# Kernel optimization log

Hardware: AMD Instinct MI355X
Metric: run time of the kernel (lower is better)

The kernel has to match this reference:

```python
import jax, jax.numpy as jnp
import numpy as np

B, T, V, E, H, L = 32, 128, 32000, 1024, 1024, 3


def lstm_layer(x, Wx, Wh, b, h0, c0):
    """Standard LSTM (i,f,g,o gate order). x: [B,T,D]. Returns ([B,T,H], (h,c))."""
    def step(carry, xt):
        h, c = carry
        z = xt @ Wx + h @ Wh + b          # [B, 4H]
        i, f, g, o = jnp.split(z, 4, axis=-1)
        c = jax.nn.sigmoid(f) * c + jax.nn.sigmoid(i) * jnp.tanh(g)
        h = jax.nn.sigmoid(o) * jnp.tanh(c)
        return (h, c), h
    (h, c), ys = jax.lax.scan(step, (h0, c0), jnp.swapaxes(x, 0, 1))
    return jnp.swapaxes(ys, 0, 1), (h, c)


def setup_inputs() -> dict:
    key = jax.random.key(0)
    ks = jax.random.split(key, 12)
    s = 0.05  # small init to avoid gate saturation
    inp = {
        "enc_ids": jax.random.randint(ks[0], (B, T), 0, V, dtype=jnp.int32),
        "dec_ids": jax.random.randint(ks[1], (B, T), 0, V, dtype=jnp.int32),
        "emb": jax.random.normal(ks[2], (V, E), jnp.float32) * s,
        "Wx_enc": jax.random.normal(ks[3], (L, E, 4 * H), jnp.float32) * s,
        "Wh_enc": jax.random.normal(ks[4], (L, H, 4 * H), jnp.float32) * s,
        "b_enc": jnp.zeros((L, 4 * H), jnp.float32),
        "Wx_dec": jax.random.normal(ks[5], (L, E, 4 * H), jnp.float32) * s,
        "Wh_dec": jax.random.normal(ks[6], (L, H, 4 * H), jnp.float32) * s,
        "b_dec": jnp.zeros((L, 4 * H), jnp.float32),
        "dense_W": jax.random.normal(ks[7], (H, V), jnp.float32) * s,
        "dense_b": jnp.zeros((V,), jnp.float32),
    }
    return inp


def reference(enc_ids, dec_ids, emb, Wx_enc, Wh_enc, b_enc, Wx_dec, Wh_dec, b_dec, dense_W, dense_b):
    zeros = jnp.zeros((B, H), jnp.float32)
    # encoder: 3 stacked LSTMs, zero initial state each
    x = emb[enc_ids]                                      # [B,T,E]
    state = (zeros, zeros)
    for l in range(L):
        x, state = lstm_layer(x, Wx_enc[l], Wh_enc[l], b_enc[l], zeros, zeros)
    # decoder: faithful to source state chaining:
    # dec layer0 init = enc layer2 final; dec layer_{i+1} init = dec layer_i final
    y = emb[dec_ids]                                      # [B,T,E]
    for l in range(L):
        y, state = lstm_layer(y, Wx_dec[l], Wh_dec[l], b_dec[l], state[0], state[1])
    logits = y.reshape(-1, H) @ dense_W + dense_b          # [B*T, V]
    return logits.reshape(B, T, V)
```

## Files before the change

kernel.cpp:

```cpp
#include <hip/hip_runtime.h>


typedef __bf16 bf8 __attribute__((ext_vector_type(8)));
typedef float  f4  __attribute__((ext_vector_type(4)));

#define TLEN  128
#define HID   1024
#define G4    4096
#define VOC   32000
#define NBLK_SEQ 64

__device__ __forceinline__ ushort f2bf(float f) {
  unsigned u = __builtin_bit_cast(unsigned, f);
  u += 0x7fffu + ((u >> 16) & 1u);
  return (ushort)(u >> 16);
}
__device__ __forceinline__ float sigmoidf_(float x) { return 1.f / (1.f + expf(-x)); }

__device__ __forceinline__ void ld16_sys(uint4& v, const void* p) {
  asm volatile("global_load_dwordx4 %0, %1, off sc0 sc1" : "=v"(v) : "v"(p));
}
__device__ __forceinline__ unsigned ld4_sys(const void* p) {
  unsigned v;
  asm volatile("global_load_dword %0, %1, off sc0 sc1\n\ts_waitcnt vmcnt(0)"
               : "=v"(v) : "v"(p) : "memory");
  return v;
}
__device__ __forceinline__ void ld4_sys3(unsigned& a, unsigned& b, unsigned& c,
                                         const void* pa, const void* pb, const void* pc) {
  asm volatile("global_load_dword %0, %3, off sc0 sc1\n\t"
               "global_load_dword %1, %4, off sc0 sc1\n\t"
               "global_load_dword %2, %5, off sc0 sc1\n\t"
               "s_waitcnt vmcnt(0)"
               : "=&v"(a), "=&v"(b), "=&v"(c)
               : "v"(pa), "v"(pb), "v"(pc) : "memory");
}
__device__ __forceinline__ void st4_sys(void* p, unsigned v) {
  asm volatile("global_store_dword %0, %1, off sc0 sc1" :: "v"(p), "v"(v) : "memory");
}
__device__ __forceinline__ void wait_vm0() {
  asm volatile("s_waitcnt vmcnt(0)" ::: "memory");
  __builtin_amdgcn_sched_barrier(0);
}

typedef const __attribute__((address_space(1))) void GvoidC;
typedef __attribute__((address_space(3))) void Lvoid;
__device__ __forceinline__ void g2l16(const void* g, void* l) {
  __builtin_amdgcn_global_load_lds((GvoidC*)g, (Lvoid*)l, 16, 0, 0);
}

__global__ __launch_bounds__(256) void embed_kernel(const int* __restrict__ ids,
    const float* __restrict__ emb, ushort* __restrict__ out) {
  int r = blockIdx.x;
  int b = r & 31, t = r >> 5;
  int id = ids[b * TLEN + t];
  const float4* src = (const float4*)(emb + (size_t)id * HID);
  float4 v = src[threadIdx.x];
  ushort4 o;
  o.x = f2bf(v.x); o.y = f2bf(v.y); o.z = f2bf(v.z); o.w = f2bf(v.w);
  *(ushort4*)(out + (size_t)r * HID + threadIdx.x * 4) = o;
}

__global__ __launch_bounds__(256) void transpose_cvt(const float* __restrict__ W,
    ushort* __restrict__ Wt, int R, int C) {
  __shared__ float tile[32][33];
  int tx = threadIdx.x & 31, ty = threadIdx.x >> 5;
  int c0 = blockIdx.x * 32, r0 = blockIdx.y * 32;
  #pragma unroll
  for (int i = 0; i < 32; i += 8)
    tile[ty + i][tx] = W[(size_t)(r0 + ty + i) * C + c0 + tx];
  __syncthreads();
  #pragma unroll
  for (int i = 0; i < 32; i += 8)
    Wt[(size_t)(c0 + ty + i) * R + r0 + tx] = f2bf(tile[tx][ty + i]);
}

__global__ __launch_bounds__(256) void gemm_bt(const ushort* __restrict__ A,
    const ushort* __restrict__ Bt, const float* __restrict__ bias,
    float* __restrict__ C, int M, int N, int K, int permute) {
  __shared__ __align__(16) ushort lA[2 * 128 * 32];
  __shared__ __align__(16) ushort lB[2 * 128 * 32];
  int tid = threadIdx.x;
  int lane = tid & 63, wave = tid >> 6;
  int nwg = gridDim.x * gridDim.y;
  int wg  = blockIdx.y * gridDim.x + blockIdx.x;
  int q   = nwg >> 3;
  int swg = (wg & 7) * q + (wg >> 3);
  int m0 = (swg / gridDim.x) * 128, n0 = (swg % gridDim.x) * 128;
  int wr = wave >> 1, wc = wave & 1;
  f4 zero = {0.f, 0.f, 0.f, 0.f};
  f4 acc[4][4];
  #pragma unroll
  for (int i = 0; i < 4; i++)
    #pragma unroll
    for (int j = 0; j < 4; j++) acc[i][j] = zero;

  const ushort* Ag = A  + (size_t)(m0 + wave * 32 + (lane >> 2)) * K + (lane & 3) * 8;
  const ushort* Bg = Bt + (size_t)(n0 + wave * 32 + (lane >> 2)) * K + (lane & 3) * 8;
  ushort* lApa = lA + wave * 1024;
  ushort* lApb = lA + 4096 + wave * 1024;
  ushort* lBpa = lB + wave * 1024;
  ushort* lBpb = lB + 4096 + wave * 1024;

  for (int kt = 0; kt < K; kt += 64) {
    g2l16(Ag + kt,                    lApa);
    g2l16(Ag + (size_t)16 * K + kt,       lApa + 512);
    g2l16(Ag + kt + 32,               lApb);
    g2l16(Ag + (size_t)16 * K + kt + 32,  lApb + 512);
    g2l16(Bg + kt,                    lBpa);
    g2l16(Bg + (size_t)16 * K + kt,       lBpa + 512);
    g2l16(Bg + kt + 32,               lBpb);
    g2l16(Bg + (size_t)16 * K + kt + 32,  lBpb + 512);
    __syncthreads();
    #pragma unroll
    for (int h = 0; h < 2; h++) {
      const ushort* ab = lA + h * 4096;
      const ushort* bb = lB + h * 4096;
      bf8 aF[4], bF[4];
      #pragma unroll
      for (int i = 0; i < 4; i++)
        aF[i] = *(const bf8*)(ab + (wr * 64 + i * 16 + (lane & 15)) * 32 + (lane >> 4) * 8);
      #pragma unroll
      for (int j = 0; j < 4; j++)
        bF[j] = *(const bf8*)(bb + (wc * 64 + j * 16 + (lane & 15)) * 32 + (lane >> 4) * 8);
      #pragma unroll
      for (int i = 0; i < 4; i++)
        #pragma unroll
        for (int j = 0; j < 4; j++)
          acc[i][j] = __builtin_amdgcn_mfma_f32_16x16x32_bf16(aF[i], bF[j], acc[i][j], 0, 0, 0);
    }
    __syncthreads();
  }
  #pragma unroll
  for (int i = 0; i < 4; i++) {
    #pragma unroll
    for (int j = 0; j < 4; j++) {
      int col = n0 + wc * 64 + j * 16 + (lane & 15);
      float bv = bias ? bias[col] : 0.f;
      #pragma unroll
      for (int v = 0; v < 4; v++) {
        int row = m0 + wr * 64 + i * 16 + (lane >> 4) * 4 + v;
        int orow = permute ? ((row & 31) * TLEN + (row >> 5)) : row;
        C[(size_t)orow * N + col] = acc[i][j][v] + bv;
      }
    }
  }
}

__global__ __launch_bounds__(512, 1) void enc_wave(
    const float*  __restrict__ Zpre,
    const ushort* __restrict__ WhT,
    const ushort* __restrict__ WxT,
    const float*  __restrict__ bE,
    ushort*       __restrict__ hxC,
    float*        __restrict__ cSe,
    ushort*       __restrict__ hS,
    unsigned*     __restrict__ flags)
{
  const int bx = blockIdx.x;
  const int l = bx >> 6, jg = bx & 63;
  const int j0 = jg * 16;
  const int tid = threadIdx.x;
  const int lane = tid & 63, wave = tid >> 6;
  const int op = wave >> 2, ks = wave & 3;
  const int rr = tid >> 4, jj = tid & 15;

  __shared__ float zp[8][4][32][17];

  float cc = cSe[(size_t)l * 32768 + rr * HID + j0 + jj];
  float bias4[4];
  #pragma unroll
  for (int g = 0; g < 4; g++)
    bias4[g] = bE[l * G4 + g * HID + j0 + jj];

  const bool mfma_on = (l > 0) || (op == 0);
  bf8 bw[4][8];
  if (mfma_on) {
    const ushort* Wb = op ? (WxT + (size_t)(l - 1) * G4 * HID)
                          : (WhT + (size_t)l * G4 * HID);
    #pragma unroll
    for (int g = 0; g < 4; g++) {
      const ushort* Bp = Wb + (size_t)(g * HID + j0 + (lane & 15)) * HID
                       + ks * 256 + (lane >> 4) * 8;
      #pragma unroll
      for (int kk = 0; kk < 8; kk++)
        bw[g][kk] = *(const bf8*)(Bp + kk * 32);
    }
  }

  const int r0 = lane & 15, r1 = r0 + 16;
  const int lk = lane >> 4;
  const int aoff0 = ks * 8192 + (lk >> 1) * 512 + r0 * 16 + (lk & 1) * 8;
  const int aoff1 = ks * 8192 + (lk >> 1) * 512 + r1 * 16 + (lk & 1) * 8;

  float zv4[4], zn4[4];
  if (l == 0) {
    #pragma unroll
    for (int g = 0; g < 4; g++)
      zv4[g] = Zpre[(size_t)rr * G4 + g * HID + j0 + jj];
  }

  for (int w = 0; w < 130; ++w) {
    if (w > 0) {
      if (wave == 0) {
        for (;;) {
          unsigned a, b, c;
          ld4_sys3(a, b, c, flags + lane * 4, flags + (64 + lane) * 4,
                   flags + (128 + lane) * 4);
          if (!__ballot(a < (unsigned)w || b < (unsigned)w || c < (unsigned)w)) break;
          __builtin_amdgcn_s_sleep(1);
        }
      }
      __syncthreads();
    }
    const int t = w - l;
    if (t >= 0 && t < TLEN) {
      uint4 ha0[8], ha1[8];
      if (mfma_on) {
        const ushort* src = (op == 0)
          ? hxC + ((size_t)l * 2 + ((t - 1) & 1)) * 32768
          : hxC + ((size_t)(l - 1) * 2 + (t & 1)) * 32768;
        #pragma unroll
        for (int kk = 0; kk < 8; kk++) {
          ld16_sys(ha0[kk], src + aoff0 + kk * 1024);
          ld16_sys(ha1[kk], src + aoff1 + kk * 1024);
        }
        wait_vm0();
      }

      if (l == 0 && t + 1 < TLEN) {
        const float* Ztn = Zpre + (size_t)(t + 1) * 32 * G4;
        #pragma unroll
        for (int g = 0; g < 4; g++)
          zn4[g] = Ztn[(size_t)rr * G4 + g * HID + j0 + jj];
      }

      if (mfma_on) {
        f4 acc0[4], acc1[4];
        #pragma unroll
        for (int g = 0; g < 4; g++) { acc0[g] = (f4){0,0,0,0}; acc1[g] = (f4){0,0,0,0}; }
        #pragma unroll
        for (int kk = 0; kk < 8; kk++) {
          bf8 a0 = __builtin_bit_cast(bf8, ha0[kk]);
          bf8 a1 = __builtin_bit_cast(bf8, ha1[kk]);
          #pragma unroll
          for (int g = 0; g < 4; g++) {
            acc0[g] = __builtin_amdgcn_mfma_f32_16x16x32_bf16(a0, bw[g][kk], acc0[g], 0, 0, 0);
            acc1[g] = __builtin_amdgcn_mfma_f32_16x16x32_bf16(a1, bw[g][kk], acc1[g], 0, 0, 0);
          }
        }
        #pragma unroll
        for (int g = 0; g < 4; g++)
          #pragma unroll
          for (int v = 0; v < 4; v++) {
            zp[wave][g][(lane >> 4) * 4 + v][lane & 15]      = acc0[g][v];
            zp[wave][g][16 + (lane >> 4) * 4 + v][lane & 15] = acc1[g][v];
          }
      }
      __syncthreads();

      float z[4];
      #pragma unroll
      for (int g = 0; g < 4; g++) {
        float s = zp[0][g][rr][jj] + zp[1][g][rr][jj]
                + zp[2][g][rr][jj] + zp[3][g][rr][jj];
        if (l > 0)
          s += zp[4][g][rr][jj] + zp[5][g][rr][jj]
             + zp[6][g][rr][jj] + zp[7][g][rr][jj] + bias4[g];
        else
          s += zv4[g];
        z[g] = s;
      }
      if (l == 0) {
        #pragma unroll
        for (int g = 0; g < 4; g++) zv4[g] = zn4[g];
      }
      float ig = sigmoidf_(z[0]), fg = sigmoidf_(z[1]);
      float gv = tanhf(z[2]),     og = sigmoidf_(z[3]);
      cc = fg * cc + ig * gv;
      float hv = og * tanhf(cc);
      ushort hb = f2bf(hv);
      unsigned u = (unsigned)hb;
      unsigned nb = __shfl_xor(u, 1);
      if ((jj & 1) == 0)
        st4_sys(hxC + ((size_t)l * 2 + (t & 1)) * 32768 + jg * 512 + rr * 16 + jj,
                u | (nb << 16));
      if (t == TLEN - 1) {
        hS [(size_t)l * 32768 + rr * HID + j0 + jj] = hb;
        cSe[(size_t)l * 32768 + rr * HID + j0 + jj] = cc;
      }
      wait_vm0();
    }
    __syncthreads();
    if (tid == 0) st4_sys(flags + bx * 4, (unsigned)(w + 1));
  }
}

__global__ __launch_bounds__(256, 1) void lstm_seq(
    const float*  __restrict__ Zpre,
    const ushort* __restrict__ Wht,
    float*        __restrict__ cS,
    ushort*       __restrict__ yout,
    ushort*       __restrict__ hx,
    unsigned*     __restrict__ flags,
    unsigned fbase)
{
  const int jg = blockIdx.x;
  const int j0 = jg * 16;
  const int tid = threadIdx.x;
  const int lane = tid & 63, wave = tid >> 6;
  const int rr = tid >> 3, cp = tid & 7;

  __shared__ float zp[4][4][32][17];

  float2 cc = *(const float2*)(cS + (size_t)rr * HID + j0 + 2 * cp);

  bf8 bw[4][8];
  #pragma unroll
  for (int g = 0; g < 4; g++) {
    const ushort* Bp = Wht + (size_t)(g * HID + j0 + (lane & 15)) * HID
                     + wave * 256 + (lane >> 4) * 8;
    #pragma unroll
    for (int kk = 0; kk < 8; kk++)
      bw[g][kk] = *(const bf8*)(Bp + kk * 32);
  }

  const int r0 = lane & 15, r1 = r0 + 16;
  const int lk = lane >> 4;
  const int aoff0 = wave * 8192 + (lk >> 1) * 512 + r0 * 16 + (lk & 1) * 8;
  const int aoff1 = wave * 8192 + (lk >> 1) * 512 + r1 * 16 + (lk & 1) * 8;

  float2 zv[4], zn[4];
  #pragma unroll
  for (int g = 0; g < 4; g++)
    zv[g] = *(const float2*)(Zpre + (size_t)rr * G4 + g * HID + j0 + 2 * cp);

  for (int t = 0; t < TLEN; ++t) {
    if (t > 0) {
      const unsigned* fp = flags + lane * 4;
      const unsigned want = fbase + (unsigned)t;
      while (__ballot(ld4_sys(fp) < want)) {}
    }
    const ushort* hsrc = hx + ((t + 1) & 1) * 32768;
    uint4 ha0[8], ha1[8];
    #pragma unroll
    for (int kk = 0; kk < 8; kk++) {
      ld16_sys(ha0[kk], hsrc + aoff0 + kk * 1024);
      ld16_sys(ha1[kk], hsrc + aoff1 + kk * 1024);
    }
    wait_vm0();

    if (t + 1 < TLEN) {
      const float* Ztn = Zpre + (size_t)(t + 1) * 32 * G4;
      #pragma unroll
      for (int g = 0; g < 4; g++)
        zn[g] = *(const float2*)(Ztn + (size_t)rr * G4 + g * HID + j0 + 2 * cp);
    }

    f4 acc0[4], acc1[4];
    #pragma unroll
    for (int g = 0; g < 4; g++) { acc0[g] = (f4){0,0,0,0}; acc1[g] = (f4){0,0,0,0}; }
    #pragma unroll
    for (int kk = 0; kk < 8; kk++) {
      bf8 a0 = __builtin_bit_cast(bf8, ha0[kk]);
      bf8 a1 = __builtin_bit_cast(bf8, ha1[kk]);
      #pragma unroll
      for (int g = 0; g < 4; g++) {
        acc0[g] = __builtin_amdgcn_mfma_f32_16x16x32_bf16(a0, bw[g][kk], acc0[g], 0, 0, 0);
        acc1[g] = __builtin_amdgcn_mfma_f32_16x16x32_bf16(a1, bw[g][kk], acc1[g], 0, 0, 0);
      }
    }
    #pragma unroll
    for (int g = 0; g < 4; g++)
      #pragma unroll
      for (int v = 0; v < 4; v++) {
        zp[wave][g][(lane >> 4) * 4 + v][lane & 15]      = acc0[g][v];
        zp[wave][g][16 + (lane >> 4) * 4 + v][lane & 15] = acc1[g][v];
      }
    __syncthreads();

    float zx[4], zy[4];
    #pragma unroll
    for (int g = 0; g < 4; g++) {
      zx[g] = zv[g].x + zp[0][g][rr][2 * cp]     + zp[1][g][rr][2 * cp]
                      + zp[2][g][rr][2 * cp]     + zp[3][g][rr][2 * cp];
      zy[g] = zv[g].y + zp[0][g][rr][2 * cp + 1] + zp[1][g][rr][2 * cp + 1]
                      + zp[2][g][rr][2 * cp + 1] + zp[3][g][rr][2 * cp + 1];
    }
    cc.x = sigmoidf_(zx[1]) * cc.x + sigmoidf_(zx[0]) * tanhf(zx[2]);
    cc.y = sigmoidf_(zy[1]) * cc.y + sigmoidf_(zy[0]) * tanhf(zy[2]);
    float hv0 = sigmoidf_(zx[3]) * tanhf(cc.x);
    float hv1 = sigmoidf_(zy[3]) * tanhf(cc.y);
    unsigned packed = (unsigned)f2bf(hv0) | ((unsigned)f2bf(hv1) << 16);
    *(unsigned*)(yout + (size_t)t * 32768 + rr * HID + j0 + 2 * cp) = packed;
    st4_sys(hx + (size_t)(t & 1) * 32768 + jg * 512 + rr * 16 + 2 * cp, packed);
    #pragma unroll
    for (int g = 0; g < 4; g++) zv[g] = zn[g];

    wait_vm0();
    __syncthreads();
    if (tid == 0) st4_sys(flags + jg * 4, fbase + (unsigned)(t + 1));
  }
  *(float2*)(cS + (size_t)rr * HID + j0 + 2 * cp) = cc;
}

__global__ __launch_bounds__(256) void prep_enc(ushort* hxC, float* cSe,
                                                unsigned* flags) {
  int i = blockIdx.x * 256 + threadIdx.x;
  hxC[i] = 0;
  if (i < 98304) cSe[i] = 0.f;
  if (i < 192)   flags[i * 4] = 0;
}
__global__ __launch_bounds__(256) void prep_dec0(const ushort* __restrict__ hS2,
                                                 const float* __restrict__ cSe2,
                                                 float* cS, ushort* hx,
                                                 unsigned* flags) {
  int i = blockIdx.x * 256 + threadIdx.x;
  int row = i >> 10, col = i & 1023;
  hx[32768 + (col >> 4) * 512 + row * 16 + (col & 15)] = hS2[i];
  cS[i] = cSe2[i];
  if (i < NBLK_SEQ) flags[i * 4] = 0;
}

extern "C" void kernel_launch(void* const* d_in, const int* in_sizes, int n_in,
                              void* d_out, int out_size, void* d_ws, size_t ws_size,
                              hipStream_t stream) {
  const int*   enc_ids = (const int*)d_in[0];
  const int*   dec_ids = (const int*)d_in[1];
  const float* emb     = (const float*)d_in[2];
  const float* Wx_enc  = (const float*)d_in[3];
  const float* Wh_enc  = (const float*)d_in[4];
  const float* b_enc   = (const float*)d_in[5];
  const float* Wx_dec  = (const float*)d_in[6];
  const float* Wh_dec  = (const float*)d_in[7];
  const float* b_dec   = (const float*)d_in[8];
  const float* dense_W = (const float*)d_in[9];
  const float* dense_b = (const float*)d_in[10];
  float* out = (float*)d_out;

  char* ws = (char*)d_ws;
  const size_t SZ_BUF = (size_t)4096 * 1024 * 2;
  ushort*   bufA   = (ushort*)(ws);
  ushort*   bufB   = (ushort*)(ws + SZ_BUF);
  ushort*   Wxt    = (ushort*)(ws + 2 * SZ_BUF);
  ushort*   Wht    = (ushort*)(ws + 3 * SZ_BUF);
  ushort*   dWt    = (ushort*)(ws + 4 * SZ_BUF);
  char*     p2     = ws + 4 * SZ_BUF + (size_t)VOC * 1024 * 2;
  float*    cS     = (float*)(p2 + (size_t)32 * 1024 * 2);
  unsigned* flags  = (unsigned*)(p2 + (size_t)32 * 1024 * 2 + (size_t)32 * 1024 * 4);

  char* ob = (char*)d_out;
  float*    Zpre   = out;
  ushort*   WhTe   = (ushort*)(ob + (size_t)64  * 1024 * 1024);
  ushort*   WxTe   = (ushort*)(ob + (size_t)88  * 1024 * 1024);
  char*     st     = ob + (size_t)112 * 1024 * 1024;
  ushort*   hxC    = (ushort*)st;
  float*    cSe    = (float*)(st + 393216);
  ushort*   hS     = (ushort*)(st + 786432);
  unsigned* flags2 = (unsigned*)(st + 983040);
  ushort*   hxD    = (ushort*)(ob + (size_t)120 * 1024 * 1024);
  const size_t WSTRIDE = (size_t)G4 * HID;

  transpose_cvt<<<dim3(VOC / 32, 1024 / 32), 256, 0, stream>>>(dense_W, dWt, 1024, VOC);

  embed_kernel<<<4096, 256, 0, stream>>>(enc_ids, emb, bufA);
  transpose_cvt<<<dim3(G4 / 32, 32), 256, 0, stream>>>(Wx_enc, Wxt, 1024, G4);
  gemm_bt<<<dim3(G4 / 128, 4096 / 128), 256, 0, stream>>>(bufA, Wxt, b_enc,
                                                          Zpre, 4096, G4, 1024, 0);
  for (int l = 0; l < 3; l++)
    transpose_cvt<<<dim3(G4 / 32, 32), 256, 0, stream>>>(Wh_enc + (size_t)l * 1024 * G4,
                                                         WhTe + l * WSTRIDE, 1024, G4);
  for (int l = 1; l < 3; l++)
    transpose_cvt<<<dim3(G4 / 32, 32), 256, 0, stream>>>(Wx_enc + (size_t)l * 1024 * G4,
                                                         WxTe + (l - 1) * WSTRIDE, 1024, G4);
  prep_enc<<<768, 256, 0, stream>>>(hxC, cSe, flags2);
  enc_wave<<<192, 512, 0, stream>>>(Zpre, WhTe, WxTe, b_enc, hxC, cSe, hS, flags2);

  embed_kernel<<<4096, 256, 0, stream>>>(dec_ids, emb, bufA);
  ushort* cur = bufA; ushort* oth = bufB;
  for (int l = 0; l < 3; l++) {
    transpose_cvt<<<dim3(G4 / 32, 32), 256, 0, stream>>>(Wx_dec + (size_t)l * 1024 * G4, Wxt, 1024, G4);
    transpose_cvt<<<dim3(G4 / 32, 32), 256, 0, stream>>>(Wh_dec + (size_t)l * 1024 * G4, Wht, 1024, G4);
    gemm_bt<<<dim3(G4 / 128, 4096 / 128), 256, 0, stream>>>(cur, Wxt, b_dec + (size_t)l * G4,
                                                            Zpre, 4096, G4, 1024, 0);
    if (l == 0)
      prep_dec0<<<128, 256, 0, stream>>>(hS + 2 * 32768, cSe + 2 * 32768, cS, hxD, flags);
    lstm_seq<<<NBLK_SEQ, 256, 0, stream>>>(Zpre, Wht, cS, oth, hxD, flags,
                                           (unsigned)(l * TLEN));
    ushort* tmp = cur; cur = oth; oth = tmp;
  }

  gemm_bt<<<dim3(VOC / 128, 4096 / 128), 256, 0, stream>>>(cur, dWt, dense_b, out,
                                                           4096, VOC, 1024, 1);
}
```

Before: 3.009 ms.

## Overlap next decoder layer's input projection with the recurrent LSTM sweep

The decoder LSTM kernel now launches 128 extra helper blocks beside the 64 recurrent blocks. Each helper waits on the per-timestep flags, then computes the next layer's Wx projection plus bias from the freshly produced hidden state, using MFMA with a swizzled LDS tile. This replaces the separate input-projection GEMM launches for decoder layers 1 and 2, so that work runs on otherwise idle CUs while the sequential recurrence proceeds. To support this, hidden states are kept for every timestep instead of a double buffer, Zpre ping-pongs between two buffers, and the decoder Wx transposes are hoisted ahead of the encoder. The risk is extra memory traffic and spinning competing with the latency-critical recurrent blocks, and the scheme relies on all 192 blocks being co-resident.

```diff
diff --git a/kernel.cpp b/kernel.cpp
--- a/kernel.cpp
+++ b/kernel.cpp
@@ -301,17 +301,83 @@
     const ushort* __restrict__ Wht,
     float*        __restrict__ cS,
     ushort*       __restrict__ yout,
-    ushort*       __restrict__ hx,
+    ushort*       __restrict__ hxAll,
     unsigned*     __restrict__ flags,
-    unsigned fbase)
+    unsigned fbase, int h0slot,
+    const ushort* __restrict__ WxTn,
+    const float*  __restrict__ bn,
+    float*        __restrict__ Zout)
 {
-  const int jg = blockIdx.x;
-  const int j0 = jg * 16;
+  const int bx = blockIdx.x;
   const int tid = threadIdx.x;
   const int lane = tid & 63, wave = tid >> 6;
+
+  __shared__ float zp[4][4][32][17];
+  __shared__ __align__(16) char aLDS[65536];
+
+  if (bx >= 64) {
+    const int hb = bx - 64;
+    const int n0 = (hb & 31) * 128;
+    const int tq = hb >> 5;
+    const int colA = n0 + wave * 32 + (lane & 15);
+    const int colB = colA + 16;
+    const float biasA = bn[colA], biasB = bn[colB];
+    const ushort* BpA = WxTn + (size_t)colA * HID + (lane >> 4) * 8;
+    const ushort* BpB = WxTn + (size_t)colB * HID + (lane >> 4) * 8;
+    const int r0 = lane & 15, r1 = r0 + 16;
+    const int klb = (lane >> 4) * 16;
+    const int swz = (r0 & 7) << 4;
+    for (int t = tq * 32; t < tq * 32 + 32; ++t) {
+      if (wave == 0) {
+        const unsigned* fp = flags + lane * 4;
+        const unsigned want = fbase + (unsigned)t + 1;
+        while (__ballot(ld4_sys(fp) < want)) __builtin_amdgcn_s_sleep(8);
+      }
+      __syncthreads();
+      const char* src = (const char*)(hxAll + (size_t)t * 32768);
+      uint4 hreg[16];
+      #pragma unroll
+      for (int it = 0; it < 16; it++)
+        ld16_sys(hreg[it], src + (size_t)(tid + it * 256) * 16);
+      wait_vm0();
+      #pragma unroll
+      for (int it = 0; it < 16; it++) {
+        int b = (tid + it * 256) * 16;
+        int off = b & 1023;
+        int row = off >> 5;
+        int kbyte = (b >> 10) * 32 + (off & 31);
+        *(uint4*)(aLDS + row * 2048 + (kbyte ^ ((row & 7) << 4))) = hreg[it];
+      }
+      __syncthreads();
+      f4 acc00 = {0,0,0,0}, acc01 = {0,0,0,0}, acc10 = {0,0,0,0}, acc11 = {0,0,0,0};
+      #pragma unroll 8
+      for (int kt = 0; kt < HID; kt += 32) {
+        int cb = kt * 2 + klb;
+        bf8 a0 = *(const bf8*)(aLDS + r0 * 2048 + (cb ^ swz));
+        bf8 a1 = *(const bf8*)(aLDS + r1 * 2048 + (cb ^ swz));
+        bf8 b0 = *(const bf8*)(BpA + kt);
+        bf8 b1 = *(const bf8*)(BpB + kt);
+        acc00 = __builtin_amdgcn_mfma_f32_16x16x32_bf16(a0, b0, acc00, 0, 0, 0);
+        acc10 = __builtin_amdgcn_mfma_f32_16x16x32_bf16(a1, b0, acc10, 0, 0, 0);
+        acc01 = __builtin_amdgcn_mfma_f32_16x16x32_bf16(a0, b1, acc01, 0, 0, 0);
+        acc11 = __builtin_amdgcn_mfma_f32_16x16x32_bf16(a1, b1, acc11, 0, 0, 0);
+      }
+      #pragma unroll
+      for (int v = 0; v < 4; v++) {
+        int ra = t * 32 + (lane >> 4) * 4 + v;
+        int rb = ra + 16;
+        Zout[(size_t)ra * G4 + colA] = acc00[v] + biasA;
+        Zout[(size_t)ra * G4 + colB] = acc01[v] + biasB;
+        Zout[(size_t)rb * G4 + colA] = acc10[v] + biasA;
+        Zout[(size_t)rb * G4 + colB] = acc11[v] + biasB;
+      }
+    }
+    return;
+  }
+
+  const int jg = bx;
+  const int j0 = jg * 16;
   const int rr = tid >> 3, cp = tid & 7;
-
-  __shared__ float zp[4][4][32][17];
 
   float2 cc = *(const float2*)(cS + (size_t)rr * HID + j0 + 2 * cp);
 
@@ -341,7 +407,7 @@
       const unsigned want = fbase + (unsigned)t;
       while (__ballot(ld4_sys(fp) < want)) {}
     }
-    const ushort* hsrc = hx + ((t + 1) & 1) * 32768;
+    const ushort* hsrc = hxAll + (size_t)(t == 0 ? h0slot : (t - 1)) * 32768;
     uint4 ha0[8], ha1[8];
     #pragma unroll
     for (int kk = 0; kk < 8; kk++) {
@@ -393,7 +459,7 @@
     float hv1 = sigmoidf_(zy[3]) * tanhf(cc.y);
     unsigned packed = (unsigned)f2bf(hv0) | ((unsigned)f2bf(hv1) << 16);
     *(unsigned*)(yout + (size_t)t * 32768 + rr * HID + j0 + 2 * cp) = packed;
-    st4_sys(hx + (size_t)(t & 1) * 32768 + jg * 512 + rr * 16 + 2 * cp, packed);
+    st4_sys(hxAll + (size_t)t * 32768 + jg * 512 + rr * 16 + 2 * cp, packed);
     #pragma unroll
     for (int g = 0; g < 4; g++) zv[g] = zn[g];
 
@@ -413,11 +479,11 @@
 }
 __global__ __launch_bounds__(256) void prep_dec0(const ushort* __restrict__ hS2,
                                                  const float* __restrict__ cSe2,
-                                                 float* cS, ushort* hx,
+                                                 float* cS, ushort* hxAll,
                                                  unsigned* flags) {
   int i = blockIdx.x * 256 + threadIdx.x;
   int row = i >> 10, col = i & 1023;
-  hx[32768 + (col >> 4) * 512 + row * 16 + (col & 15)] = hS2[i];
+  hxAll[(size_t)128 * 32768 + (col >> 4) * 512 + row * 16 + (col & 15)] = hS2[i];
   cS[i] = cSe2[i];
   if (i < NBLK_SEQ) flags[i * 4] = 0;
 }
@@ -450,7 +516,7 @@
   unsigned* flags  = (unsigned*)(p2 + (size_t)32 * 1024 * 2 + (size_t)32 * 1024 * 4);
 
   char* ob = (char*)d_out;
-  float*    Zpre   = out;
+  float*    ZpreA  = out;
   ushort*   WhTe   = (ushort*)(ob + (size_t)64  * 1024 * 1024);
   ushort*   WxTe   = (ushort*)(ob + (size_t)88  * 1024 * 1024);
   char*     st     = ob + (size_t)112 * 1024 * 1024;
@@ -458,7 +524,9 @@
   float*    cSe    = (float*)(st + 393216);
   ushort*   hS     = (ushort*)(st + 786432);
   unsigned* flags2 = (unsigned*)(st + 983040);
-  ushort*   hxD    = (ushort*)(ob + (size_t)120 * 1024 * 1024);
+  ushort*   hxAll  = (ushort*)(ob + (size_t)120 * 1024 * 1024);
+  float*    ZpreB  = (float*)(ob + (size_t)160 * 1024 * 1024);
+  ushort*   WxTD   = (ushort*)(ob + (size_t)240 * 1024 * 1024);
   const size_t WSTRIDE = (size_t)G4 * HID;
 
   transpose_cvt<<<dim3(VOC / 32, 1024 / 32), 256, 0, stream>>>(dense_W, dWt, 1024, VOC);
@@ -466,30 +534,42 @@
   embed_kernel<<<4096, 256, 0, stream>>>(enc_ids, emb, bufA);
   transpose_cvt<<<dim3(G4 / 32, 32), 256, 0, stream>>>(Wx_enc, Wxt, 1024, G4);
   gemm_bt<<<dim3(G4 / 128, 4096 / 128), 256, 0, stream>>>(bufA, Wxt, b_enc,
-                                                          Zpre, 4096, G4, 1024, 0);
+                                                          ZpreA, 4096, G4, 1024, 0);
   for (int l = 0; l < 3; l++)
     transpose_cvt<<<dim3(G4 / 32, 32), 256, 0, stream>>>(Wh_enc + (size_t)l * 1024 * G4,
                                                          WhTe + l * WSTRIDE, 1024, G4);
   for (int l = 1; l < 3; l++)
     transpose_cvt<<<dim3(G4 / 32, 32), 256, 0, stream>>>(Wx_enc + (size_t)l * 1024 * G4,
                                                          WxTe + (l - 1) * WSTRIDE, 1024, G4);
+  for (int l = 1; l < 3; l++)
+    transpose_cvt<<<dim3(G4 / 32, 32), 256, 0, stream>>>(Wx_dec + (size_t)l * 1024 * G4,
+                                                         WxTD + (l - 1) * WSTRIDE, 1024, G4);
   prep_enc<<<768, 256, 0, stream>>>(hxC, cSe, flags2);
-  enc_wave<<<192, 512, 0, stream>>>(Zpre, WhTe, WxTe, b_enc, hxC, cSe, hS, flags2);
+  enc_wave<<<192, 512, 0, stream>>>(ZpreA, WhTe, WxTe, b_enc, hxC, cSe, hS, flags2);
 
   embed_kernel<<<4096, 256, 0, stream>>>(dec_ids, emb, bufA);
-  ushort* cur = bufA; ushort* oth = bufB;
+  transpose_cvt<<<dim3(G4 / 32, 32), 256, 0, stream>>>(Wx_dec, Wxt, 1024, G4);
+  gemm_bt<<<dim3(G4 / 128, 4096 / 128), 256, 0, stream>>>(bufA, Wxt, b_dec,
+                                                          ZpreA, 4096, G4, 1024, 0);
+  prep_dec0<<<128, 256, 0, stream>>>(hS + 2 * 32768, cSe + 2 * 32768, cS, hxAll, flags);
   for (int l = 0; l < 3; l++) {
-    transpose_cvt<<<dim3(G4 / 32, 32), 256, 0, stream>>>(Wx_dec + (size_t)l * 1024 * G4, Wxt, 1024, G4);
-    transpose_cvt<<<dim3(G4 / 32, 32), 256, 0, stream>>>(Wh_dec + (size_t)l * 1024 * G4, Wht, 1024, G4);
-    gemm_bt<<<dim3(G4 / 128, 4096 / 128), 256, 0, stream>>>(cur, Wxt, b_dec + (size_t)l * G4,
-                                                            Zpre, 4096, G4, 1024, 0);
-    if (l == 0)
-      prep_dec0<<<128, 256, 0, stream>>>(hS + 2 * 32768, cSe + 2 * 32768, cS, hxD, flags);
-    lstm_seq<<<NBLK_SEQ, 256, 0, stream>>>(Zpre, Wht, cS, oth, hxD, flags,
-                                           (unsigned)(l * TLEN));
-    ushort* tmp = cur; cur = oth; oth = tmp;
-  }
-
-  gemm_bt<<<dim3(VOC / 128, 4096 / 128), 256, 0, stream>>>(cur, dWt, dense_b, out,
+    transpose_cvt<<<dim3(G4 / 32, 32), 256, 0, stream>>>(Wh_dec + (size_t)l * 1024 * G4,
+                                                         Wht, 1024, G4);
+    const float* Zread = (l == 1) ? ZpreB : ZpreA;
+    if (l < 2) {
+      float* Zo = (l == 0) ? ZpreB : ZpreA;
+      lstm_seq<<<192, 256, 0, stream>>>(Zread, Wht, cS, bufA, hxAll, flags,
+                                        (unsigned)(l * TLEN), l == 0 ? 128 : 127,
+                                        WxTD + (size_t)l * WSTRIDE,
+                                        b_dec + (size_t)(l + 1) * G4, Zo);
+    } else {
+      lstm_seq<<<64, 256, 0, stream>>>(Zread, Wht, cS, bufA, hxAll, flags,
+                                       (unsigned)(l * TLEN), 127,
+                                       (const ushort*)nullptr, (const float*)nullptr,
+                                       (float*)nullptr);
+    }
+  }
+
+  gemm_bt<<<dim3(VOC / 128, 4096 / 128), 256, 0, stream>>>(bufA, dWt, dense_b, out,
                                                            4096, VOC, 1024, 1);
 }
```

Result: slower. 3.302 ms (+9.7%).
